# Kernel tuning notes

Measured on AMD Instinct MI355X. Metric: run time of the kernel, lower is better.

Reference implementation:

```python
import jax, jax.numpy as jnp
import numpy as np

DIM = 768
HEADS = 12
HEAD_DIM = DIM // HEADS
HIDDEN = 4 * DIM
SCALE = HEAD_DIM ** -0.5
LN_EPS = 1e-5


def layer_norm(x, g, b):
    mu = jnp.mean(x, axis=-1, keepdims=True)
    var = jnp.var(x, axis=-1, keepdims=True)
    return (x - mu) * jax.lax.rsqrt(var + LN_EPS) * g + b


def setup_inputs() -> dict:
    key = jax.random.key(0)
    ks = jax.random.split(key, 10)
    B, N = 2, 2048
    s = 0.02
    return {
        "x": jax.random.normal(ks[0], (B, N, DIM), jnp.float32),
        "elevation": jax.random.uniform(ks[1], (B, N), jnp.float32),
        "qkv_w": jax.random.normal(ks[2], (DIM, 3 * DIM), jnp.float32) * s,
        "qkv_b": jnp.zeros((3 * DIM,), jnp.float32),
        "proj_w": jax.random.normal(ks[3], (DIM, DIM), jnp.float32) * s,
        "proj_b": jnp.zeros((DIM,), jnp.float32),
        "ln1_g": jnp.ones((DIM,), jnp.float32),
        "ln1_b": jnp.zeros((DIM,), jnp.float32),
        "ln2_g": jnp.ones((DIM,), jnp.float32),
        "ln2_b": jnp.zeros((DIM,), jnp.float32),
        "fc1_w": jax.random.normal(ks[4], (DIM, HIDDEN), jnp.float32) * s,
        "fc1_b": jnp.zeros((HIDDEN,), jnp.float32),
        "fc2_w": jax.random.normal(ks[5], (HIDDEN, DIM), jnp.float32) * s,
        "fc2_b": jnp.zeros((DIM,), jnp.float32),
        "barrier": jnp.asarray(3.0, jnp.float32),
    }


def reference(x, elevation, qkv_w, qkv_b, proj_w, proj_b, ln1_g, ln1_b,
              ln2_g, ln2_b, fc1_w, fc1_b, fc2_w, fc2_b, barrier):
    B, N, C = x.shape
    h = layer_norm(x, ln1_g, ln1_b)
    qkv = (h @ qkv_w + qkv_b).reshape(B, N, 3, HEADS, HEAD_DIM)
    q, k, v = jnp.moveaxis(qkv, 2, 0)  # each [B, N, H, D]
    # scores: [B, H, N, N]
    scores = jnp.einsum('bnhd,bmhd->bhnm', q, k) * SCALE
    w = jax.nn.softmax(scores, axis=-1)
    # pairwise elevation mask [B, N, N]: sigmoid(-s * (elev_j - elev_i))
    diff = elevation[:, None, :] - elevation[:, :, None]
    mask = jnp.clip(jax.nn.sigmoid(-barrier * diff), 1e-6, 1.0)
    w = w * mask[:, None, :, :]
    w = w / (jnp.sum(w, axis=-1, keepdims=True) + 1e-8)
    attn_out = jnp.einsum('bhnm,bmhd->bnhd', w, v).reshape(B, N, C)
    x = x + attn_out @ proj_w + proj_b
    h2 = layer_norm(x, ln2_g, ln2_b)
    mlp = jax.nn.gelu(h2 @ fc1_w + fc1_b, approximate=False) @ fc2_w + fc2_b
    return x + mlp
```

## Files before the change

### kernel.cpp

```cpp
#include <hip/hip_runtime.h>
#include <math.h>

#define DIM 768
#define HEADS 12
#define SEQ 2048
#define ROWS 4096
#define LN_EPS 1e-5f

typedef __attribute__((ext_vector_type(8))) short short8;
typedef __attribute__((ext_vector_type(4))) float floatx4;
typedef __attribute__((ext_vector_type(16))) float floatx16;
typedef unsigned short ushort_t;

__device__ __forceinline__ ushort_t f2bf(float x) {
    unsigned u = __float_as_uint(x);
    u += 0x7fff + ((u >> 16) & 1);
    return (ushort_t)(u >> 16);
}

__device__ __forceinline__ void gload_lds16(const void* g, void* l) {
    __builtin_amdgcn_global_load_lds((const __attribute__((address_space(1))) void*)g,
                                     (__attribute__((address_space(3))) void*)l, 16, 0, 0);
}

__launch_bounds__(256)
__global__ void wconv_all(const float* __restrict__ w0, const float* __restrict__ w1,
                          const float* __restrict__ w2, const float* __restrict__ w3,
                          ushort_t* __restrict__ t0, ushort_t* __restrict__ t1,
                          ushort_t* __restrict__ t2, ushort_t* __restrict__ t3) {
    __shared__ __align__(16) ushort_t s[64][72];
    int bid = blockIdx.x;
    const float* W; ushort_t* WT; int K, N, nx, id;
    if (bid < 432)       { W = w0; WT = t0; K = 768;  N = 2304; nx = 36; id = bid; }
    else if (bid < 576)  { W = w1; WT = t1; K = 768;  N = 768;  nx = 12; id = bid - 432; }
    else if (bid < 1152) { W = w2; WT = t2; K = 768;  N = 3072; nx = 48; id = bid - 576; }
    else                 { W = w3; WT = t3; K = 3072; N = 768;  nx = 12; id = bid - 1152; }
    int tx = id % nx, ty = id / nx;
    int k0 = ty * 64, n0 = tx * 64;
    int t = threadIdx.x;
    int rr0 = t >> 4, c4 = (t & 15) * 4;
    for (int rr = rr0; rr < 64; rr += 16) {
        float4 w = *(const float4*)(W + (size_t)(k0 + rr) * N + n0 + c4);
        s[c4 + 0][rr] = f2bf(w.x); s[c4 + 1][rr] = f2bf(w.y);
        s[c4 + 2][rr] = f2bf(w.z); s[c4 + 3][rr] = f2bf(w.w);
    }
    __syncthreads();
    int nl = t >> 2, kq = (t & 3) * 16;
    uint4 a = *(const uint4*)&s[nl][kq];
    uint4 b = *(const uint4*)&s[nl][kq + 8];
    *(uint4*)(WT + (size_t)(n0 + nl) * K + k0 + kq) = a;
    *(uint4*)(WT + (size_t)(n0 + nl) * K + k0 + kq + 8) = b;
}

__launch_bounds__(256)
__global__ void gelev_kernel(const float* __restrict__ elev, const float* __restrict__ barrier_p,
                             float* __restrict__ G, float* __restrict__ C2) {
    int i = blockIdx.x * 256 + threadIdx.x;
    float be = barrier_p[0] * elev[i];
    G[i]  = __expf(be);
    C2[i] = be;
}

__launch_bounds__(256)
__global__ void ln_kernel(const float* __restrict__ x, const float* __restrict__ g,
                          const float* __restrict__ b, ushort_t* __restrict__ out) {
    int row = blockIdx.x;
    const float* xr = x + (size_t)row * DIM;
    int t = threadIdx.x;
    float v0 = xr[t], v1 = xr[t + 256], v2 = xr[t + 512];
    float s  = v0 + v1 + v2;
    float ss = v0 * v0 + v1 * v1 + v2 * v2;
    #pragma unroll
    for (int o = 32; o >= 1; o >>= 1) { s += __shfl_xor(s, o); ss += __shfl_xor(ss, o); }
    __shared__ float rs[4], rss[4];
    int wid = t >> 6, lane = t & 63;
    if (lane == 0) { rs[wid] = s; rss[wid] = ss; }
    __syncthreads();
    if (t == 0) {
        float S = 0.f, SS = 0.f;
        for (int i = 0; i < 4; i++) { S += rs[i]; SS += rss[i]; }
        rs[0] = S; rss[0] = SS;
    }
    __syncthreads();
    float mean = rs[0] * (1.0f / DIM);
    float var  = rss[0] * (1.0f / DIM) - mean * mean;
    float rstd = rsqrtf(var + LN_EPS);
    ushort_t* orow = out + (size_t)row * DIM;
    orow[t]       = f2bf((v0 - mean) * rstd * g[t]       + b[t]);
    orow[t + 256] = f2bf((v1 - mean) * rstd * g[t + 256] + b[t + 256]);
    orow[t + 512] = f2bf((v2 - mean) * rstd * g[t + 512] + b[t + 512]);
}

template<int EPI>
__launch_bounds__(256)
__global__ void gemm32(const ushort_t* __restrict__ A, const ushort_t* __restrict__ WT,
                       const float* __restrict__ bias, ushort_t* __restrict__ outB,
                       ushort_t* __restrict__ qb, ushort_t* __restrict__ kb,
                       ushort_t* __restrict__ vb, int N, int K) {
    __shared__ __align__(16) ushort_t sA[128 * 32];
    __shared__ __align__(16) ushort_t sB[128 * 32];
    int t = threadIdx.x;
    int row0 = blockIdx.y * 128, col0 = blockIdx.x * 128;
    int wid = t >> 6, lane = t & 63, l31 = lane & 31, hb = lane >> 5;
    int wm = wid >> 1, wn = wid & 1;

    floatx16 acc[2][2];
    #pragma unroll
    for (int i = 0; i < 2; i++)
        #pragma unroll
        for (int j = 0; j < 2; j++)
            #pragma unroll
            for (int e = 0; e < 16; e++) acc[i][j][e] = 0.f;

    for (int k0 = 0; k0 < K; k0 += 32) {
        #pragma unroll
        for (int i = 0; i < 2; i++) {
            int c = i * 256 + t;
            int r = c >> 2, blk = c & 3;
            gload_lds16(A  + (size_t)(row0 + r) * K + k0 + ((blk ^ (r & 3)) << 3), &sA[c * 8]);
            gload_lds16(WT + (size_t)(col0 + r) * K + k0 + ((blk ^ (r & 3)) << 3), &sB[c * 8]);
        }
        __syncthreads();
        #pragma unroll
        for (int s = 0; s < 2; s++) {
            int blk = s * 2 + hb;
            int ra0 = wm * 64 + l31, ra1 = ra0 + 32;
            int rb0 = wn * 64 + l31, rb1 = rb0 + 32;
            short8 a0 = *(const short8*)&sA[ra0 * 32 + ((blk ^ (ra0 & 3)) << 3)];
            short8 a1 = *(const short8*)&sA[ra1 * 32 + ((blk ^ (ra1 & 3)) << 3)];
            short8 b0 = *(const short8*)&sB[rb0 * 32 + ((blk ^ (rb0 & 3)) << 3)];
            short8 b1 = *(const short8*)&sB[rb1 * 32 + ((blk ^ (rb1 & 3)) << 3)];
            acc[0][0] = __builtin_amdgcn_mfma_f32_32x32x16_bf16(a0, b0, acc[0][0], 0, 0, 0);
            acc[0][1] = __builtin_amdgcn_mfma_f32_32x32x16_bf16(a0, b1, acc[0][1], 0, 0, 0);
            acc[1][0] = __builtin_amdgcn_mfma_f32_32x32x16_bf16(a1, b0, acc[1][0], 0, 0, 0);
            acc[1][1] = __builtin_amdgcn_mfma_f32_32x32x16_bf16(a1, b1, acc[1][1], 0, 0, 0);
        }
        __syncthreads();
    }

    #pragma unroll
    for (int mt = 0; mt < 2; mt++) {
        #pragma unroll
        for (int nt = 0; nt < 2; nt++) {
            int gcol = col0 + wn * 64 + nt * 32 + l31;
            float bv = bias[gcol];
            if (EPI == 0) {
                int which = gcol / 768;
                int hc = gcol - which * 768;
                int hh = hc >> 6, d = hc & 63;
                #pragma unroll
                for (int rg = 0; rg < 16; rg++) {
                    int grow = row0 + wm * 64 + mt * 32 + (rg & 3) + 8 * (rg >> 2) + 4 * hb;
                    float v = acc[mt][nt][rg] + bv;
                    int b_ = grow >> 11, n = grow & 2047;
                    size_t bhh = (size_t)(b_ * 12 + hh);
                    if (which == 0)      qb[(bhh * 2048 + n) * 64 + d] = f2bf(v * 0.125f);
                    else if (which == 1) kb[(bhh * 2048 + n) * 64 + d] = f2bf(v);
                    else                 vb[(bhh * 64 + d) * 2048 + n] = f2bf(v);
                }
            } else {
                #pragma unroll
                for (int rg = 0; rg < 16; rg++) {
                    int grow = row0 + wm * 64 + mt * 32 + (rg & 3) + 8 * (rg >> 2) + 4 * hb;
                    float v = acc[mt][nt][rg] + bv;
                    v = 0.5f * v * (1.f + erff(v * 0.70710678118654752f));
                    outB[(size_t)grow * N + gcol] = f2bf(v);
                }
            }
        }
    }
}

template<int BN, int EPI>
__launch_bounds__(256)
__global__ void gemm_bf16(const ushort_t* __restrict__ A, const ushort_t* __restrict__ WT,
                          const float* __restrict__ bias, const float* __restrict__ res,
                          float* __restrict__ outF, int N, int K) {
    constexpr int NT = BN / 32;
    __shared__ __align__(16) ushort_t sA[64 * 32];
    __shared__ __align__(16) ushort_t sB[BN * 32];
    int t = threadIdx.x;
    int row0 = blockIdx.y * 64, col0 = blockIdx.x * BN;
    int wid = t >> 6, lane = t & 63;
    int wm = wid >> 1, wn = wid & 1;
    int cl = lane & 15, quad = lane >> 4;

    floatx4 acc[2][NT];
    #pragma unroll
    for (int i = 0; i < 2; i++)
        #pragma unroll
        for (int j = 0; j < NT; j++) { floatx4 z = {0.f, 0.f, 0.f, 0.f}; acc[i][j] = z; }

    for (int k0 = 0; k0 < K; k0 += 32) {
        {
            int r = t >> 2, sub = t & 3;
            gload_lds16(A + (size_t)(row0 + r) * K + k0 + sub * 8, &sA[t * 8]);
        }
        #pragma unroll
        for (int i = 0; i < BN / 64; i++) {
            int c = i * 256 + t;
            int r = c >> 2, sub = c & 3;
            gload_lds16(WT + (size_t)(col0 + r) * K + k0 + sub * 8, &sB[c * 8]);
        }
        __syncthreads();
        short8 a[2], b[NT];
        #pragma unroll
        for (int i = 0; i < 2; i++)
            a[i] = *(const short8*)&sA[(wm * 32 + i * 16 + cl) * 32 + quad * 8];
        #pragma unroll
        for (int j = 0; j < NT; j++)
            b[j] = *(const short8*)&sB[(wn * (BN / 2) + j * 16 + cl) * 32 + quad * 8];
        #pragma unroll
        for (int i = 0; i < 2; i++)
            #pragma unroll
            for (int j = 0; j < NT; j++)
                acc[i][j] = __builtin_amdgcn_mfma_f32_16x16x32_bf16(a[i], b[j], acc[i][j], 0, 0, 0);
        __syncthreads();
    }

    #pragma unroll
    for (int i = 0; i < 2; i++) {
        #pragma unroll
        for (int j = 0; j < NT; j++) {
            int gcol = col0 + wn * (BN / 2) + j * 16 + cl;
            float bv = bias[gcol];
            #pragma unroll
            for (int rg = 0; rg < 4; rg++) {
                int grow = row0 + wm * 32 + i * 16 + quad * 4 + rg;
                float v = acc[i][j][rg] + bv + res[(size_t)grow * N + gcol];
                outF[(size_t)grow * N + gcol] = v;
            }
        }
    }
}


#define PREFETCH(K0N, KSN, VTN)                                                   \
    {                                                                             \
        const ushort_t* kbase_ = kb + (bh * 2048 + (K0N)) * 64;                   \
        const ushort_t* vbase_ = vb + bh * 131072 + (K0N);                        \
        int c0_ = t, r0_ = c0_ >> 3, b0_ = c0_ & 7;                               \
        gload_lds16(kbase_ + (r0_ << 6) + ((b0_ ^ (r0_ & 7)) << 3), &KSN[c0_ * 8]); \
        gload_lds16(vbase_ + (size_t)r0_ * 2048 + ((b0_ ^ (r0_ & 7)) << 3), &VTN[c0_ * 8]); \
        int c1_ = 256 + t, r1_ = c1_ >> 3, b1_ = c1_ & 7;                         \
        gload_lds16(kbase_ + (r1_ << 6) + ((b1_ ^ (r1_ & 7)) << 3), &KSN[c1_ * 8]); \
        gload_lds16(vbase_ + (size_t)r1_ * 2048 + ((b1_ ^ (r1_ & 7)) << 3), &VTN[c1_ * 8]); \
    }

#define ATTN_TILE(KT, KSC, VTC, KSN, VTN)                                         \
    {                                                                             \
        __syncthreads();                                                          \
        if ((KT) < 31) PREFETCH(((KT) + 1) * 64, KSN, VTN)                        \
        float gjv_[4];                                                            \
        gjv_[0] = G[b * 2048 + (KT) * 64 + cl];                                   \
        gjv_[1] = G[b * 2048 + (KT) * 64 + 16 + cl];                              \
        gjv_[2] = G[b * 2048 + (KT) * 64 + 32 + cl];                              \
        gjv_[3] = G[b * 2048 + (KT) * 64 + 48 + cl];                              \
        floatx4 s_[4];                                                            \
        s_[0] = c2init; s_[1] = c2init; s_[2] = c2init; s_[3] = c2init;           \
        _Pragma("unroll")                                                         \
        for (int kh = 0; kh < 2; kh++) {                                          \
            short8 aq_ = *(const short8*)&Qs[((wid * 16 + cl) << 6) + (((kh * 4 + quad) ^ (cl & 7)) << 3)]; \
            _Pragma("unroll")                                                     \
            for (int nt = 0; nt < 4; nt++) {                                      \
                short8 bk_ = *(const short8*)&KSC[((nt * 16 + cl) << 6) + (((kh * 4 + quad) ^ (cl & 7)) << 3)]; \
                s_[nt] = __builtin_amdgcn_mfma_f32_16x16x32_bf16(aq_, bk_, s_[nt], 0, 0, 0); \
            }                                                                     \
        }                                                                         \
        _Pragma("unroll")                                                         \
        for (int rg = 0; rg < 4; rg++) {                                          \
            int prow_ = wid * 16 + quad * 4 + rg;                                 \
            int r8_ = prow_ & 7, pb_ = prow_ << 6, cs_ = cl & 7, ch_ = cl >> 3;   \
            _Pragma("unroll")                                                     \
            for (int nt = 0; nt < 4; nt++) {                                      \
                float tf_ = __expf(s_[nt][rg]);                                   \
                float p_  = tf_ * __builtin_amdgcn_rcpf(gi[rg] + gjv_[nt]);       \
                sem[rg] += p_;                                                    \
                Ps[pb_ + (((nt * 2 + ch_) ^ r8_) << 3) + cs_] = (ushort_t)(__float_as_uint(p_) >> 16); \
            }                                                                     \
        }                                                                         \
        _Pragma("unroll")                                                         \
        for (int kh = 0; kh < 2; kh++) {                                          \
            short8 ap_ = *(const short8*)&Ps[((wid * 16 + cl) << 6) + (((kh * 4 + quad) ^ (cl & 7)) << 3)]; \
            _Pragma("unroll")                                                     \
            for (int dt = 0; dt < 4; dt++) {                                      \
                short8 bv_ = *(const short8*)&VTC[((dt * 16 + cl) << 6) + (((kh * 4 + quad) ^ (cl & 7)) << 3)]; \
                o[dt] = __builtin_amdgcn_mfma_f32_16x16x32_bf16(ap_, bv_, o[dt], 0, 0, 0); \
            }                                                                     \
        }                                                                         \
    }

__launch_bounds__(256)
__global__ void attn_mfma(const ushort_t* __restrict__ qb, const ushort_t* __restrict__ kb,
                          const ushort_t* __restrict__ vb, const float* __restrict__ G,
                          const float* __restrict__ C2, ushort_t* __restrict__ attn) {
    __shared__ __align__(16) ushort_t Qs[4096];
    __shared__ __align__(16) ushort_t Ks0[4096];
    __shared__ __align__(16) ushort_t Ks1[4096];
    __shared__ __align__(16) ushort_t Vt0[4096];
    __shared__ __align__(16) ushort_t Vt1[4096];
    __shared__ __align__(16) ushort_t Ps[4096];
    int qt = blockIdx.x, h = blockIdx.y, b = blockIdx.z;
    int t = threadIdx.x, wid = t >> 6, lane = t & 63;
    int cl = lane & 15, quad = lane >> 4;
    int q0 = qt * 64;
    size_t bh = (size_t)(b * 12 + h);

    const ushort_t* qbase = qb + (bh * 2048 + q0) * 64;
    #pragma unroll
    for (int i = 0; i < 2; i++) {
        int c = i * 256 + t, row = c >> 3, blk = c & 7;
        gload_lds16(qbase + (row << 6) + ((blk ^ (row & 7)) << 3), &Qs[c * 8]);
    }
    int qrow4 = b * 2048 + q0 + wid * 16 + quad * 4;
    float4 g4  = *(const float4*)(G  + qrow4);
    float4 c24 = *(const float4*)(C2 + qrow4);
    float gi[4]  = {g4.x, g4.y, g4.z, g4.w};
    floatx4 c2init = {c24.x, c24.y, c24.z, c24.w};

    PREFETCH(0, Ks0, Vt0)

    floatx4 o[4];
    #pragma unroll
    for (int j = 0; j < 4; j++) { floatx4 z = {0.f, 0.f, 0.f, 0.f}; o[j] = z; }
    float sem[4] = {0.f, 0.f, 0.f, 0.f};

    for (int kt = 0; kt < 32; kt += 2) {
        ATTN_TILE(kt,     Ks0, Vt0, Ks1, Vt1)
        ATTN_TILE(kt + 1, Ks1, Vt1, Ks0, Vt0)
    }

    #pragma unroll
    for (int rg = 0; rg < 4; rg++) {
        float m = sem[rg];
        #pragma unroll
        for (int off = 1; off < 16; off <<= 1) m += __shfl_xor(m, off);
        float inv = __builtin_amdgcn_rcpf(m);
        int grow = b * 2048 + q0 + wid * 16 + quad * 4 + rg;
        #pragma unroll
        for (int dt = 0; dt < 4; dt++)
            attn[(size_t)grow * 768 + h * 64 + dt * 16 + cl] = f2bf(o[dt][rg] * inv);
    }
}

extern "C" void kernel_launch(void* const* d_in, const int* in_sizes, int n_in,
                              void* d_out, int out_size, void* d_ws, size_t ws_size,
                              hipStream_t stream) {
    const float* x      = (const float*)d_in[0];
    const float* elev   = (const float*)d_in[1];
    const float* qkv_w  = (const float*)d_in[2];
    const float* qkv_b  = (const float*)d_in[3];
    const float* proj_w = (const float*)d_in[4];
    const float* proj_b = (const float*)d_in[5];
    const float* ln1_g  = (const float*)d_in[6];
    const float* ln1_b  = (const float*)d_in[7];
    const float* ln2_g  = (const float*)d_in[8];
    const float* ln2_b  = (const float*)d_in[9];
    const float* fc1_w  = (const float*)d_in[10];
    const float* fc1_b  = (const float*)d_in[11];
    const float* fc2_w  = (const float*)d_in[12];
    const float* fc2_b  = (const float*)d_in[13];
    const float* barrier= (const float*)d_in[14];
    float* out = (float*)d_out;
    char* ws = (char*)d_ws;

    ushort_t* h    = (ushort_t*)(ws + 0);
    ushort_t* qb   = (ushort_t*)(ws + 6291456);
    ushort_t* kb   = (ushort_t*)(ws + 12582912);
    ushort_t* vb   = (ushort_t*)(ws + 18874368);
    ushort_t* f1   = (ushort_t*)(ws + 0);
    ushort_t* attn = (ushort_t*)(ws + 25165824);
    ushort_t* h2   = (ushort_t*)(ws + 31457280);
    float*    Gf   = (float*)(ws + 31457280);
    float*    C2f  = (float*)(ws + 31473664);
    ushort_t* qkvT = (ushort_t*)(ws + 37748736);
    ushort_t* projT= (ushort_t*)(ws + 41287680);
    ushort_t* fc1T = (ushort_t*)(ws + 42467328);
    ushort_t* fc2T = (ushort_t*)(ws + 47185920);

    wconv_all<<<1728, 256, 0, stream>>>(qkv_w, proj_w, fc1_w, fc2_w, qkvT, projT, fc1T, fc2T);
    gelev_kernel<<<16, 256, 0, stream>>>(elev, barrier, Gf, C2f);

    ln_kernel<<<ROWS, 256, 0, stream>>>(x, ln1_g, ln1_b, h);
    gemm32<0><<<dim3(2304 / 128, 32), 256, 0, stream>>>(
        h, qkvT, qkv_b, nullptr, qb, kb, vb, 2304, 768);
    attn_mfma<<<dim3(32, HEADS, 2), 256, 0, stream>>>(qb, kb, vb, Gf, C2f, attn);
    gemm_bf16<64, 2><<<dim3(768 / 64, 64), 256, 0, stream>>>(
        attn, projT, proj_b, x, out, 768, 768);
    ln_kernel<<<ROWS, 256, 0, stream>>>(out, ln2_g, ln2_b, h2);
    gemm32<1><<<dim3(3072 / 128, 32), 256, 0, stream>>>(
        h2, fc1T, fc1_b, f1, nullptr, nullptr, nullptr, 3072, 768);
    gemm_bf16<64, 2><<<dim3(768 / 64, 64), 256, 0, stream>>>(
        f1, fc2T, fc2_b, out, out, 768, 3072);
}
```

Baseline: 324.4 us.

## Double-buffer LDS tiles in GEMM kernels to overlap loads with MFMA

Both GEMM kernels now use two LDS buffers per operand and issue the async global-to-LDS load for the next K-slice before computing on the current one. Each K step drops from two barriers to one, and memory latency can overlap with MFMA work. The cost is double the shared memory, which may reduce occupancy. gemm_bf16 loses its BN template parameter and is fixed at 64 columns, which is the only width it was launched with.

```diff
diff --git a/kernel.cpp b/kernel.cpp
--- a/kernel.cpp
+++ b/kernel.cpp
@@ -91,18 +91,49 @@
     orow[t + 512] = f2bf((v2 - mean) * rstd * g[t + 512] + b[t + 512]);
 }
 
+
+#define G32_PREFETCH(K0, SA, SB)                                                      \
+    {                                                                                 \
+        int c0_ = t, r0_ = c0_ >> 2, bl0_ = c0_ & 3;                                  \
+        gload_lds16(A  + (size_t)(row0 + r0_) * K + (K0) + ((bl0_ ^ (r0_ & 3)) << 3), &SA[c0_ * 8]); \
+        gload_lds16(WT + (size_t)(col0 + r0_) * K + (K0) + ((bl0_ ^ (r0_ & 3)) << 3), &SB[c0_ * 8]); \
+        int c1_ = 256 + t, r1_ = c1_ >> 2, bl1_ = c1_ & 3;                            \
+        gload_lds16(A  + (size_t)(row0 + r1_) * K + (K0) + ((bl1_ ^ (r1_ & 3)) << 3), &SA[c1_ * 8]); \
+        gload_lds16(WT + (size_t)(col0 + r1_) * K + (K0) + ((bl1_ ^ (r1_ & 3)) << 3), &SB[c1_ * 8]); \
+    }
+
+#define G32_COMPUTE(SA, SB)                                                           \
+    {                                                                                 \
+        _Pragma("unroll")                                                             \
+        for (int s = 0; s < 2; s++) {                                                 \
+            int blk_ = s * 2 + hb;                                                    \
+            short8 a0_ = *(const short8*)&SA[ra0 * 32 + ((blk_ ^ (ra0 & 3)) << 3)];   \
+            short8 a1_ = *(const short8*)&SA[ra1 * 32 + ((blk_ ^ (ra1 & 3)) << 3)];   \
+            short8 b0_ = *(const short8*)&SB[rb0 * 32 + ((blk_ ^ (rb0 & 3)) << 3)];   \
+            short8 b1_ = *(const short8*)&SB[rb1 * 32 + ((blk_ ^ (rb1 & 3)) << 3)];   \
+            acc[0][0] = __builtin_amdgcn_mfma_f32_32x32x16_bf16(a0_, b0_, acc[0][0], 0, 0, 0); \
+            acc[0][1] = __builtin_amdgcn_mfma_f32_32x32x16_bf16(a0_, b1_, acc[0][1], 0, 0, 0); \
+            acc[1][0] = __builtin_amdgcn_mfma_f32_32x32x16_bf16(a1_, b0_, acc[1][0], 0, 0, 0); \
+            acc[1][1] = __builtin_amdgcn_mfma_f32_32x32x16_bf16(a1_, b1_, acc[1][1], 0, 0, 0); \
+        }                                                                             \
+    }
+
 template<int EPI>
 __launch_bounds__(256)
 __global__ void gemm32(const ushort_t* __restrict__ A, const ushort_t* __restrict__ WT,
                        const float* __restrict__ bias, ushort_t* __restrict__ outB,
                        ushort_t* __restrict__ qb, ushort_t* __restrict__ kb,
                        ushort_t* __restrict__ vb, int N, int K) {
-    __shared__ __align__(16) ushort_t sA[128 * 32];
-    __shared__ __align__(16) ushort_t sB[128 * 32];
+    __shared__ __align__(16) ushort_t sA0[128 * 32];
+    __shared__ __align__(16) ushort_t sA1[128 * 32];
+    __shared__ __align__(16) ushort_t sB0[128 * 32];
+    __shared__ __align__(16) ushort_t sB1[128 * 32];
     int t = threadIdx.x;
     int row0 = blockIdx.y * 128, col0 = blockIdx.x * 128;
     int wid = t >> 6, lane = t & 63, l31 = lane & 31, hb = lane >> 5;
     int wm = wid >> 1, wn = wid & 1;
+    int ra0 = wm * 64 + l31, ra1 = ra0 + 32;
+    int rb0 = wn * 64 + l31, rb1 = rb0 + 32;
 
     floatx16 acc[2][2];
     #pragma unroll
@@ -112,30 +143,14 @@
             #pragma unroll
             for (int e = 0; e < 16; e++) acc[i][j][e] = 0.f;
 
-    for (int k0 = 0; k0 < K; k0 += 32) {
-        #pragma unroll
-        for (int i = 0; i < 2; i++) {
-            int c = i * 256 + t;
-            int r = c >> 2, blk = c & 3;
-            gload_lds16(A  + (size_t)(row0 + r) * K + k0 + ((blk ^ (r & 3)) << 3), &sA[c * 8]);
-            gload_lds16(WT + (size_t)(col0 + r) * K + k0 + ((blk ^ (r & 3)) << 3), &sB[c * 8]);
-        }
+    G32_PREFETCH(0, sA0, sB0)
+    for (int k0 = 0; k0 < K; k0 += 64) {
         __syncthreads();
-        #pragma unroll
-        for (int s = 0; s < 2; s++) {
-            int blk = s * 2 + hb;
-            int ra0 = wm * 64 + l31, ra1 = ra0 + 32;
-            int rb0 = wn * 64 + l31, rb1 = rb0 + 32;
-            short8 a0 = *(const short8*)&sA[ra0 * 32 + ((blk ^ (ra0 & 3)) << 3)];
-            short8 a1 = *(const short8*)&sA[ra1 * 32 + ((blk ^ (ra1 & 3)) << 3)];
-            short8 b0 = *(const short8*)&sB[rb0 * 32 + ((blk ^ (rb0 & 3)) << 3)];
-            short8 b1 = *(const short8*)&sB[rb1 * 32 + ((blk ^ (rb1 & 3)) << 3)];
-            acc[0][0] = __builtin_amdgcn_mfma_f32_32x32x16_bf16(a0, b0, acc[0][0], 0, 0, 0);
-            acc[0][1] = __builtin_amdgcn_mfma_f32_32x32x16_bf16(a0, b1, acc[0][1], 0, 0, 0);
-            acc[1][0] = __builtin_amdgcn_mfma_f32_32x32x16_bf16(a1, b0, acc[1][0], 0, 0, 0);
-            acc[1][1] = __builtin_amdgcn_mfma_f32_32x32x16_bf16(a1, b1, acc[1][1], 0, 0, 0);
-        }
+        if (k0 + 32 < K) G32_PREFETCH(k0 + 32, sA1, sB1)
+        G32_COMPUTE(sA0, sB0)
         __syncthreads();
+        if (k0 + 64 < K) G32_PREFETCH(k0 + 64, sA0, sB0)
+        G32_COMPUTE(sA1, sB1)
     }
 
     #pragma unroll
@@ -171,58 +186,65 @@
     }
 }
 
-template<int BN, int EPI>
+
+#define GB_PREFETCH(K0, SA, SB)                                                       \
+    {                                                                                 \
+        int r_ = t >> 2, sub_ = t & 3;                                                \
+        gload_lds16(A  + (size_t)(row0 + r_) * K + (K0) + sub_ * 8, &SA[t * 8]);      \
+        gload_lds16(WT + (size_t)(col0 + r_) * K + (K0) + sub_ * 8, &SB[t * 8]);      \
+    }
+
+#define GB_COMPUTE(SA, SB)                                                            \
+    {                                                                                 \
+        short8 a_[2], b_[2];                                                          \
+        _Pragma("unroll")                                                             \
+        for (int i = 0; i < 2; i++)                                                   \
+            a_[i] = *(const short8*)&SA[(wm * 32 + i * 16 + cl) * 32 + quad * 8];     \
+        _Pragma("unroll")                                                             \
+        for (int j = 0; j < 2; j++)                                                   \
+            b_[j] = *(const short8*)&SB[(wn * 32 + j * 16 + cl) * 32 + quad * 8];     \
+        _Pragma("unroll")                                                             \
+        for (int i = 0; i < 2; i++)                                                   \
+            _Pragma("unroll")                                                         \
+            for (int j = 0; j < 2; j++)                                               \
+                acc[i][j] = __builtin_amdgcn_mfma_f32_16x16x32_bf16(a_[i], b_[j], acc[i][j], 0, 0, 0); \
+    }
+
 __launch_bounds__(256)
 __global__ void gemm_bf16(const ushort_t* __restrict__ A, const ushort_t* __restrict__ WT,
                           const float* __restrict__ bias, const float* __restrict__ res,
                           float* __restrict__ outF, int N, int K) {
-    constexpr int NT = BN / 32;
-    __shared__ __align__(16) ushort_t sA[64 * 32];
-    __shared__ __align__(16) ushort_t sB[BN * 32];
+    __shared__ __align__(16) ushort_t sA0[64 * 32];
+    __shared__ __align__(16) ushort_t sA1[64 * 32];
+    __shared__ __align__(16) ushort_t sB0[64 * 32];
+    __shared__ __align__(16) ushort_t sB1[64 * 32];
     int t = threadIdx.x;
-    int row0 = blockIdx.y * 64, col0 = blockIdx.x * BN;
+    int row0 = blockIdx.y * 64, col0 = blockIdx.x * 64;
     int wid = t >> 6, lane = t & 63;
     int wm = wid >> 1, wn = wid & 1;
     int cl = lane & 15, quad = lane >> 4;
 
-    floatx4 acc[2][NT];
+    floatx4 acc[2][2];
     #pragma unroll
     for (int i = 0; i < 2; i++)
         #pragma unroll
-        for (int j = 0; j < NT; j++) { floatx4 z = {0.f, 0.f, 0.f, 0.f}; acc[i][j] = z; }
-
-    for (int k0 = 0; k0 < K; k0 += 32) {
-        {
-            int r = t >> 2, sub = t & 3;
-            gload_lds16(A + (size_t)(row0 + r) * K + k0 + sub * 8, &sA[t * 8]);
-        }
-        #pragma unroll
-        for (int i = 0; i < BN / 64; i++) {
-            int c = i * 256 + t;
-            int r = c >> 2, sub = c & 3;
-            gload_lds16(WT + (size_t)(col0 + r) * K + k0 + sub * 8, &sB[c * 8]);
-        }
+        for (int j = 0; j < 2; j++) { floatx4 z = {0.f, 0.f, 0.f, 0.f}; acc[i][j] = z; }
+
+    GB_PREFETCH(0, sA0, sB0)
+    for (int k0 = 0; k0 < K; k0 += 64) {
         __syncthreads();
-        short8 a[2], b[NT];
-        #pragma unroll
-        for (int i = 0; i < 2; i++)
-            a[i] = *(const short8*)&sA[(wm * 32 + i * 16 + cl) * 32 + quad * 8];
-        #pragma unroll
-        for (int j = 0; j < NT; j++)
-            b[j] = *(const short8*)&sB[(wn * (BN / 2) + j * 16 + cl) * 32 + quad * 8];
-        #pragma unroll
-        for (int i = 0; i < 2; i++)
-            #pragma unroll
-            for (int j = 0; j < NT; j++)
-                acc[i][j] = __builtin_amdgcn_mfma_f32_16x16x32_bf16(a[i], b[j], acc[i][j], 0, 0, 0);
+        if (k0 + 32 < K) GB_PREFETCH(k0 + 32, sA1, sB1)
+        GB_COMPUTE(sA0, sB0)
         __syncthreads();
+        if (k0 + 64 < K) GB_PREFETCH(k0 + 64, sA0, sB0)
+        GB_COMPUTE(sA1, sB1)
     }
 
     #pragma unroll
     for (int i = 0; i < 2; i++) {
         #pragma unroll
-        for (int j = 0; j < NT; j++) {
-            int gcol = col0 + wn * (BN / 2) + j * 16 + cl;
+        for (int j = 0; j < 2; j++) {
+            int gcol = col0 + wn * 32 + j * 16 + cl;
             float bv = bias[gcol];
             #pragma unroll
             for (int rg = 0; rg < 4; rg++) {
@@ -233,7 +255,6 @@
         }
     }
 }
-
 
 #define PREFETCH(K0N, KSN, VTN)                                                   \
     {                                                                             \
@@ -385,11 +406,11 @@
     gemm32<0><<<dim3(2304 / 128, 32), 256, 0, stream>>>(
         h, qkvT, qkv_b, nullptr, qb, kb, vb, 2304, 768);
     attn_mfma<<<dim3(32, HEADS, 2), 256, 0, stream>>>(qb, kb, vb, Gf, C2f, attn);
-    gemm_bf16<64, 2><<<dim3(768 / 64, 64), 256, 0, stream>>>(
+    gemm_bf16<<<dim3(768 / 64, 64), 256, 0, stream>>>(
         attn, projT, proj_b, x, out, 768, 768);
     ln_kernel<<<ROWS, 256, 0, stream>>>(out, ln2_g, ln2_b, h2);
     gemm32<1><<<dim3(3072 / 128, 32), 256, 0, stream>>>(
         h2, fc1T, fc1_b, f1, nullptr, nullptr, nullptr, 3072, 768);
-    gemm_bf16<64, 2><<<dim3(768 / 64, 64), 256, 0, stream>>>(
+    gemm_bf16<<<dim3(768 / 64, 64), 256, 0, stream>>>(
         f1, fc2T, fc2_b, out, out, 768, 3072);
 }
```

Result: no change. 319.9 us (-1.4%).
